# Kernel optimization log

Hardware: AMD Instinct MI355X
Metric: run time of the kernel (lower is better)

## Reference

```python
import jax, jax.numpy as jnp
import numpy as np

H = 12          # num_heads
E = 768         # key_dim
LORA_SCALE = 32.0 / 4.0  # scale / R
NEG = -1e9


def setup_inputs() -> dict:
    key = jax.random.key(0)
    ks = jax.random.split(key, 8)
    B, L = 2, 2048
    return {
        "x": jax.random.normal(ks[0], (B, L, E), jnp.float32),
        "w_in": jax.random.normal(ks[1], (E, 3 * E), jnp.float32) * 0.02,
        "b_in": jnp.zeros((3 * E,), jnp.float32),
        "A_in": jax.random.normal(ks[2], (4, 3 * E), jnp.float32) * 0.02,
        "B_in": jax.random.normal(ks[3], (E, 4), jnp.float32) * 0.02,
        "w_out": jax.random.normal(ks[4], (E, E), jnp.float32) * 0.02,
        "b_out": jnp.zeros((E,), jnp.float32),
        "A_out": jax.random.normal(ks[5], (4, E), jnp.float32) * 0.02,
        "B_out": jax.random.normal(ks[6], (E, 4), jnp.float32) * 0.02,
    }


def reference(x, w_in, b_in, A_in, B_in, w_out, b_out, A_out, B_out):
    Bb, L, _ = x.shape
    D = E // H
    # LoRA-adapted input projection: w + (scale/R) * B @ A
    w1 = w_in + LORA_SCALE * (B_in @ A_in)          # [E, 3E]
    c = jnp.einsum('ble,eo->blo', x, w1) + b_in      # [B, L, 3E]
    q, k, v = jnp.split(c, 3, axis=2)
    # split heads -> [B, H, L, D]
    def heads(t):
        return t.reshape(Bb, L, H, D).transpose(0, 2, 1, 3)
    q, k, v = heads(q), heads(k), heads(v)
    # attention scores (no 1/sqrt(d): scale=False in module defaults)
    w = jnp.einsum('bhqd,bhkd->bhqk', q, k)          # [B, H, L, L]
    band = jnp.tril(jnp.ones((L, L), jnp.float32))   # causal band
    w = w * band + NEG * (1.0 - band)
    w = jax.nn.softmax(w, axis=-1)
    a = jnp.einsum('bhqk,bhkd->bhqd', w, v)          # [B, H, L, D]
    a = a.transpose(0, 2, 1, 3).reshape(Bb, L, E)    # merge heads
    w2 = w_out + LORA_SCALE * (B_out @ A_out)        # [E, E]
    return jnp.einsum('ble,eo->blo', a, w2) + b_out
```

## Files before the change

kernel.cpp:

```cpp
#include <hip/hip_runtime.h>
#include <hip/hip_bf16.h>

#define BB 2
#define LL 2048
#define EE 768
#define HH 12
#define DD 64
#define N3 2304
#define TOK 4096
#define LOG2E 1.4426950408889634f

typedef __attribute__((ext_vector_type(8))) short short8;
typedef __attribute__((ext_vector_type(4))) float f32x4;
typedef __attribute__((ext_vector_type(4))) unsigned int uix4;
typedef unsigned int uint_t;
typedef unsigned short ushort_t;

__device__ __forceinline__ f32x4 mfma16(short8 a, short8 b, f32x4 c) {
  return __builtin_amdgcn_mfma_f32_16x16x32_bf16(a, b, c, 0, 0, 0);
}

__device__ __forceinline__ ushort_t bf16bits(float f) {
  __hip_bfloat16 h = __float2bfloat16(f);
  return *reinterpret_cast<ushort_t*>(&h);
}

__device__ __forceinline__ float bits2f(ushort_t u) {
  union { uint_t u; float f; } cv;
  cv.u = ((uint_t)u) << 16;
  return cv.f;
}

__device__ __forceinline__ void stage64(const __hip_bfloat16* gbase, int ldg,
                                        short* lds, int tid) {
  const int wave = tid >> 6, lane = tid & 63;
#pragma unroll
  for (int c = 0; c < 4; ++c) {
    int off = c * 4096 + wave * 1024 + lane * 16;
    int row = off >> 7;
    int cs  = (off & 127) >> 4;
    int cc  = cs ^ (row & 7);
    __builtin_amdgcn_global_load_lds(
        (const __attribute__((address_space(1))) void*)((const short*)gbase + (size_t)row * ldg + cc * 8),
        (__attribute__((address_space(3))) void*)(lds + c * 2048 + wave * 512),
        16, 0, 0);
  }
}

__device__ __forceinline__ void stage128(const __hip_bfloat16* gbase, int ldg,
                                         short* lds, int tid) {
  const int wave = tid >> 6, lane = tid & 63;
#pragma unroll
  for (int c = 0; c < 4; ++c) {
    int off = c * 4096 + wave * 1024 + lane * 16;
    int row = off >> 8;
    int cs  = (off & 255) >> 4;
    int cc  = cs ^ (row & 7);
    __builtin_amdgcn_global_load_lds(
        (const __attribute__((address_space(1))) void*)((const short*)gbase + (size_t)row * ldg + cc * 8),
        (__attribute__((address_space(3))) void*)(lds + c * 2048 + wave * 512),
        16, 0, 0);
  }
}

__device__ __forceinline__ short8 frag64(const short* lds, int row, int chunk) {
  return *(const short8*)(lds + row * 64 + (chunk ^ (row & 7)) * 8);
}
__device__ __forceinline__ short8 frag128(const short* lds, int row, int chunk) {
  return *(const short8*)(lds + row * 128 + (chunk ^ (row & 7)) * 8);
}

__global__ void prep_kernel(const float* __restrict__ x, const float* __restrict__ w_in,
                            const float* __restrict__ A_in, const float* __restrict__ B_in,
                            const float* __restrict__ w_out, const float* __restrict__ A_out,
                            const float* __restrict__ B_out,
                            __hip_bfloat16* __restrict__ xb, __hip_bfloat16* __restrict__ w1T,
                            __hip_bfloat16* __restrict__ w2T) {
  __shared__ float tile[32][33];
  const int bid = blockIdx.x, t = threadIdx.x;
  if (bid < 2304) {
    const float *W, *Am, *Bm;
    __hip_bfloat16* out;
    int N, tx, ty;
    if (bid < 1728) { W = w_in;  Am = A_in;  Bm = B_in;  out = w1T; N = N3; tx = bid % 72; ty = bid / 72; }
    else { int jj = bid - 1728; W = w_out; Am = A_out; Bm = B_out; out = w2T; N = EE; tx = jj % 24; ty = jj / 24; }
    const int e0 = ty * 32, o0 = tx * 32;
    const int r = t >> 5, col = t & 31;
#pragma unroll
    for (int i = 0; i < 4; ++i)
      tile[r + i * 8][col] = W[(size_t)(e0 + r + i * 8) * N + (o0 + col)];
    __syncthreads();
    const int e = e0 + col;
    const float b0 = Bm[e * 4 + 0], b1 = Bm[e * 4 + 1], b2 = Bm[e * 4 + 2], b3 = Bm[e * 4 + 3];
#pragma unroll
    for (int i = 0; i < 4; ++i) {
      const int o = o0 + r + i * 8;
      float acc = b0 * Am[o] + b1 * Am[N + o] + b2 * Am[2 * N + o] + b3 * Am[3 * N + o];
      out[(size_t)o * EE + e] = __float2bfloat16(tile[col][r + i * 8] + 8.0f * acc);
    }
  } else {
    const int j = bid - 2304;
    const float* src = x + (size_t)j * 4096 + t * 16;
    short* dst = (short*)xb + (size_t)j * 4096 + t * 16;
#pragma unroll
    for (int half = 0; half < 2; ++half) {
      float4 a = ((const float4*)src)[half * 2];
      float4 b = ((const float4*)src)[half * 2 + 1];
      short8 v;
      v[0] = (short)bf16bits(a.x); v[1] = (short)bf16bits(a.y);
      v[2] = (short)bf16bits(a.z); v[3] = (short)bf16bits(a.w);
      v[4] = (short)bf16bits(b.x); v[5] = (short)bf16bits(b.y);
      v[6] = (short)bf16bits(b.z); v[7] = (short)bf16bits(b.w);
      ((short8*)dst)[half] = v;
    }
  }
}

template<bool F32OUT, bool QSCALE>
__global__ __launch_bounds__(256, 2) void gemm_bt(const __hip_bfloat16* __restrict__ A,
                                                  const __hip_bfloat16* __restrict__ BT,
                                                  const float* __restrict__ bias,
                                                  void* __restrict__ outp,
                                                  int M, int N, int K) {
  __shared__ __align__(16) short Al[128 * 64];
  __shared__ __align__(16) short Bl[128 * 64];
  const int tid = threadIdx.x, lane = tid & 63, wave = tid >> 6;
  const int quad = lane >> 4, c16 = lane & 15;
  const int n0 = blockIdx.x * 128, m0 = blockIdx.y * 128;
  const int msub = (wave & 1) * 64, nsub = (wave >> 1) * 64;
  f32x4 acc[4][4] = {};
  for (int k0 = 0; k0 < K; k0 += 64) {
    __syncthreads();
    stage64(A + (size_t)m0 * K + k0, K, Al, tid);
    stage64(BT + (size_t)n0 * K + k0, K, Bl, tid);
    __syncthreads();
#pragma unroll
    for (int ks = 0; ks < 2; ++ks) {
      short8 af[4], bfr[4];
#pragma unroll
      for (int i = 0; i < 4; ++i) {
        af[i]  = frag64(Al, msub + i * 16 + c16, ks * 4 + quad);
        bfr[i] = frag64(Bl, nsub + i * 16 + c16, ks * 4 + quad);
      }
#pragma unroll
      for (int mi = 0; mi < 4; ++mi)
#pragma unroll
        for (int ni = 0; ni < 4; ++ni)
          acc[mi][ni] = mfma16(af[mi], bfr[ni], acc[mi][ni]);
    }
  }
#pragma unroll
  for (int ni = 0; ni < 4; ++ni) {
    int n = n0 + nsub + ni * 16 + c16;
    float bv = bias[n];
    float sc = (QSCALE && n < EE) ? LOG2E : 1.0f;
#pragma unroll
    for (int mi = 0; mi < 4; ++mi) {
      int row0 = m0 + msub + mi * 16 + quad * 4;
#pragma unroll
      for (int r = 0; r < 4; ++r) {
        float v = (acc[mi][ni][r] + bv) * sc;
        if (F32OUT) ((float*)outp)[(size_t)(row0 + r) * N + n] = v;
        else ((__hip_bfloat16*)outp)[(size_t)(row0 + r) * N + n] = __float2bfloat16(v);
      }
    }
  }
}

__global__ void vtrans_kernel(const __hip_bfloat16* __restrict__ qkv,
                              __hip_bfloat16* __restrict__ vT) {
  const int tid = threadIdx.x, lane = tid & 63, wave = tid >> 6;
  const int blk = blockIdx.x;
  const int bh = blk >> 6, lt = blk & 63;
  const int b = bh / HH, h = bh % HH;
  const int l0 = lt * 32 + wave * 8;
  const int i = lane >> 3, o = lane & 7;
  const short* src = (const short*)qkv + (size_t)(b * LL + l0 + i) * N3 + 2 * EE + h * DD + o * 8;
  uix4 u = *(const uix4*)src;
  {
    uix4 ov;
#pragma unroll
    for (int k = 0; k < 4; ++k) ov[k] = (uint_t)__shfl_xor((int)u[k], 8);
#pragma unroll
    for (int k = 0; k < 4; ++k)
      u[k] = ((i & 1) == 0) ? ((u[k] & 0xFFFFu) | (ov[k] << 16))
                            : ((ov[k] >> 16) | (u[k] & 0xFFFF0000u));
  }
  {
    uix4 ov;
#pragma unroll
    for (int k = 0; k < 4; ++k) ov[k] = (uint_t)__shfl_xor((int)u[k], 16);
    uint_t a0 = ((i & 2) == 0) ? u[0] : ov[1];
    uint_t a1 = ((i & 2) == 0) ? ov[0] : u[1];
    uint_t a2 = ((i & 2) == 0) ? u[2] : ov[3];
    uint_t a3 = ((i & 2) == 0) ? ov[2] : u[3];
    u[0] = a0; u[1] = a1; u[2] = a2; u[3] = a3;
  }
  {
    uix4 ov;
#pragma unroll
    for (int k = 0; k < 4; ++k) ov[k] = (uint_t)__shfl_xor((int)u[k], 32);
    uint_t a0 = ((i & 4) == 0) ? u[0] : ov[2];
    uint_t a1 = ((i & 4) == 0) ? u[1] : ov[3];
    uint_t a2 = ((i & 4) == 0) ? ov[0] : u[2];
    uint_t a3 = ((i & 4) == 0) ? ov[1] : u[3];
    u[0] = a0; u[1] = a1; u[2] = a2; u[3] = a3;
  }
  short* dst = (short*)vT + (size_t)((b * HH + h) * DD + o * 8 + i) * LL + l0;
  *(uix4*)dst = u;
}

#define SLOT_BYTES 8448
__global__ __launch_bounds__(256, 4) void attn_kernel(const __hip_bfloat16* __restrict__ qkv,
                                                      const __hip_bfloat16* __restrict__ vT,
                                                      char* __restrict__ Opart) {
  __shared__ __align__(16) short Kl[128 * 64];
  __shared__ __align__(16) short Vl[64 * 128];
  const int tid = threadIdx.x, lane = tid & 63, wave = tid >> 6;
  const int quad = lane >> 4, c16 = lane & 15;
  const int bid = blockIdx.x;
  const int bh = bid % 24;
  const int j = bid / 24;
  int qt, cch;
  if (j < 16)      { qt = 16 + j; cch = 0; }
  else if (j < 32) { qt = 47 - j; cch = 1; }
  else             { qt = 47 - j; cch = 0; }
  const int b = bh / HH, h = bh % HH;
  const int q0 = qt * 64;
  const int qw = q0 + wave * 16;
  const int ks = cch * 1024;
  const int ke = min((qt + 1) * 64, ks + 1024);
  short8 qf[2];
  {
    const short* qrow = (const short*)qkv + (size_t)(b * LL + qw + c16) * N3 + h * DD;
    qf[0] = *(const short8*)(qrow + quad * 8);
    qf[1] = *(const short8*)(qrow + 32 + quad * 8);
  }
  float l_i = 0.f;
  f32x4 oaccT[4] = {};
  const int srcA = ((lane >> 4) & 1) * 32 + c16;
  const int srcB = srcA + 16;
  const bool hi2 = (quad >> 1) != 0;
  for (int k0 = ks; k0 < ke; k0 += 128) {
    __syncthreads();
    stage64(qkv + (size_t)(b * LL + k0) * N3 + EE + h * DD, N3, Kl, tid);
    stage128(vT + (size_t)((b * HH + h) * DD) * LL + k0, LL, Vl, tid);
    __syncthreads();
    int nlim = (qw + 15 - k0) / 16 + 1;
    if (nlim > 8) nlim = 8;
    uint_t pkx[8], pky[8];
#pragma unroll
    for (int nt = 0; nt < 8; ++nt) {
      if (nt < nlim) {
        f32x4 a = {};
        a = mfma16(frag64(Kl, nt * 16 + c16, quad), qf[0], a);
        a = mfma16(frag64(Kl, nt * 16 + c16, 4 + quad), qf[1], a);
        if (k0 + nt * 16 + 15 > qw) {
          const int kb = k0 + nt * 16 + quad * 4;
          const int q = qw + c16;
#pragma unroll
          for (int r = 0; r < 4; ++r)
            if (kb + r > q) a[r] = -1e9f;
        }
        float p0 = exp2f(a[0]), p1 = exp2f(a[1]);
        float p2 = exp2f(a[2]), p3 = exp2f(a[3]);
        l_i += (p0 + p1) + (p2 + p3);
        pkx[nt] = (uint_t)bf16bits(p0) | ((uint_t)bf16bits(p1) << 16);
        pky[nt] = (uint_t)bf16bits(p2) | ((uint_t)bf16bits(p3) << 16);
      } else { pkx[nt] = 0; pky[nt] = 0; }
    }
    const int klim = (nlim + 1) >> 1;
#pragma unroll
    for (int kc = 0; kc < 4; ++kc) {
      if (kc < klim) {
        const int nt0 = 2 * kc, nt1 = 2 * kc + 1;
        uint_t a0 = (uint_t)__shfl((int)pkx[nt0], srcA);
        uint_t a1 = (uint_t)__shfl((int)pky[nt0], srcA);
        uint_t a2 = (uint_t)__shfl((int)pkx[nt0], srcB);
        uint_t a3 = (uint_t)__shfl((int)pky[nt0], srcB);
        uint_t b0 = (uint_t)__shfl((int)pkx[nt1], srcA);
        uint_t b1 = (uint_t)__shfl((int)pky[nt1], srcA);
        uint_t b2 = (uint_t)__shfl((int)pkx[nt1], srcB);
        uint_t b3 = (uint_t)__shfl((int)pky[nt1], srcB);
        union { uix4 u; short8 s8; } bf;
        bf.u[0] = hi2 ? b0 : a0;
        bf.u[1] = hi2 ? b1 : a1;
        bf.u[2] = hi2 ? b2 : a2;
        bf.u[3] = hi2 ? b3 : a3;
#pragma unroll
        for (int dt = 0; dt < 4; ++dt)
          oaccT[dt] = mfma16(frag128(Vl, dt * 16 + c16, kc * 4 + quad), bf.s8, oaccT[dt]);
      }
    }
  }
  float l_full = l_i;
  l_full += __shfl_xor(l_full, 16);
  l_full += __shfl_xor(l_full, 32);
  char* op = Opart + (size_t)((bh * 32 + qt) * 2 + cch) * SLOT_BYTES;
  __syncthreads();
  short* reg = Kl + wave * 1152;
#pragma unroll
  for (int dt = 0; dt < 4; ++dt) {
    uint_t w0 = (uint_t)bf16bits(oaccT[dt][0]) | ((uint_t)bf16bits(oaccT[dt][1]) << 16);
    uint_t w1 = (uint_t)bf16bits(oaccT[dt][2]) | ((uint_t)bf16bits(oaccT[dt][3]) << 16);
    uint_t* p = (uint_t*)(reg + c16 * 72 + dt * 16 + quad * 4);
    p[0] = w0; p[1] = w1;
  }
  if (quad == 0) ((float*)(op + 8192))[wave * 16 + c16] = l_full;
#pragma unroll
  for (int it = 0; it < 2; ++it) {
    int idx = it * 64 + lane;
    int tq = idx >> 3, c = idx & 7;
    short8 v = *(const short8*)(reg + tq * 72 + c * 8);
    *(short8*)((short*)op + (wave * 16 + tq) * 64 + c * 8) = v;
  }
}

__global__ void merge_kernel(const char* __restrict__ Opart,
                             __hip_bfloat16* __restrict__ abuf) {
  const int t = threadIdx.x;
  const int bh = blockIdx.x >> 5, qt = blockIdx.x & 31;
  const int b = bh / HH, h = bh % HH;
  const char* p0 = Opart + (size_t)((bh * 32 + qt) * 2) * SLOT_BYTES;
  const char* p1 = p0 + SLOT_BYTES;
  const bool two = (qt >= 16);
  const int q = t >> 2, dc = (t & 3) * 16;
  float l = ((const float*)(p0 + 8192))[q];
  if (two) l += ((const float*)(p1 + 8192))[q];
  const float inv = 1.0f / l;
  const short* o0 = (const short*)p0 + q * 64 + dc;
  const short* o1 = (const short*)p1 + q * 64 + dc;
  short8 r0[2], r1[2];
  r0[0] = *(const short8*)(o0);
  r0[1] = *(const short8*)(o0 + 8);
  if (two) { r1[0] = *(const short8*)(o1); r1[1] = *(const short8*)(o1 + 8); }
  __align__(16) short out[16];
#pragma unroll
  for (int i = 0; i < 16; ++i) {
    float v = bits2f((ushort_t)r0[i >> 3][i & 7]);
    if (two) v += bits2f((ushort_t)r1[i >> 3][i & 7]);
    out[i] = (short)bf16bits(v * inv);
  }
  short* dst = (short*)abuf + (size_t)(b * LL + qt * 64 + q) * EE + h * DD + dc;
  *(short8*)dst = *(short8*)(out);
  *(short8*)(dst + 8) = *(short8*)(out + 8);
}

extern "C" void kernel_launch(void* const* d_in, const int* in_sizes, int n_in,
                              void* d_out, int out_size, void* d_ws, size_t ws_size,
                              hipStream_t stream) {
  (void)in_sizes; (void)n_in; (void)out_size; (void)ws_size;
  const float* x     = (const float*)d_in[0];
  const float* w_in  = (const float*)d_in[1];
  const float* b_in  = (const float*)d_in[2];
  const float* A_in  = (const float*)d_in[3];
  const float* B_in  = (const float*)d_in[4];
  const float* w_out = (const float*)d_in[5];
  const float* b_out = (const float*)d_in[6];
  const float* A_out = (const float*)d_in[7];
  const float* B_out = (const float*)d_in[8];
  char* ws = (char*)d_ws;
  __hip_bfloat16* xb   = (__hip_bfloat16*)(ws);
  __hip_bfloat16* w1T  = (__hip_bfloat16*)(ws + 6291456);
  __hip_bfloat16* w2T  = (__hip_bfloat16*)(ws + 9830400);
  __hip_bfloat16* qkv  = (__hip_bfloat16*)(ws + 11010048);
  __hip_bfloat16* vT   = (__hip_bfloat16*)(ws + 29884416);
  __hip_bfloat16* abuf = (__hip_bfloat16*)(ws + 36175872);
  char* Opart          = ws + 42467328;

  prep_kernel<<<3072, 256, 0, stream>>>(x, w_in, A_in, B_in, w_out, A_out, B_out,
                                        xb, w1T, w2T);
  gemm_bt<false, true><<<dim3(N3 / 128, TOK / 128), 256, 0, stream>>>(xb, w1T, b_in, qkv, TOK, N3, EE);
  vtrans_kernel<<<BB * HH * 64, 256, 0, stream>>>(qkv, vT);
  attn_kernel<<<24 * 48, 256, 0, stream>>>(qkv, vT, Opart);
  merge_kernel<<<24 * 32, 256, 0, stream>>>(Opart, abuf);
  gemm_bt<true, false><<<dim3(EE / 128, TOK / 128), 256, 0, stream>>>(abuf, w2T, b_out, d_out, TOK, EE, EE);
}
```

Measured before the change: 171.8 us.

## Process 128-query tiles per block with two 16-row query groups per wave

The attention kernel now gives each wave 32 query rows as two 16-row sub-tiles, so each K and V fragment read from LDS is reused for both. Block count and merge grid are halved to match. The PV product now uses the 16x16x16 bf16 MFMA with P fed straight from registers, which removes the cross-lane shuffles that repacked P. In exchange there are fewer blocks to fill the GPU, more registers per wave, and causal imbalance inside each 128-row tile.

```diff
diff --git a/kernel.cpp b/kernel.cpp
--- a/kernel.cpp
+++ b/kernel.cpp
@@ -11,6 +11,7 @@
 #define LOG2E 1.4426950408889634f
 
 typedef __attribute__((ext_vector_type(8))) short short8;
+typedef __attribute__((ext_vector_type(4))) short s16x4;
 typedef __attribute__((ext_vector_type(4))) float f32x4;
 typedef __attribute__((ext_vector_type(4))) unsigned int uix4;
 typedef unsigned int uint_t;
@@ -18,6 +19,9 @@
 
 __device__ __forceinline__ f32x4 mfma16(short8 a, short8 b, f32x4 c) {
   return __builtin_amdgcn_mfma_f32_16x16x32_bf16(a, b, c, 0, 0, 0);
+}
+__device__ __forceinline__ f32x4 mfma16k16(s16x4 a, s16x4 b, f32x4 c) {
+  return __builtin_amdgcn_mfma_f32_16x16x16bf16_1k(a, b, c, 0, 0, 0);
 }
 
 __device__ __forceinline__ ushort_t bf16bits(float f) {
@@ -65,9 +69,6 @@
 
 __device__ __forceinline__ short8 frag64(const short* lds, int row, int chunk) {
   return *(const short8*)(lds + row * 64 + (chunk ^ (row & 7)) * 8);
-}
-__device__ __forceinline__ short8 frag128(const short* lds, int row, int chunk) {
-  return *(const short8*)(lds + row * 128 + (chunk ^ (row & 7)) * 8);
 }
 
 __global__ void prep_kernel(const float* __restrict__ x, const float* __restrict__ w_in,
@@ -210,7 +211,9 @@
   *(uix4*)dst = u;
 }
 
-#define SLOT_BYTES 8448
+#define SLOT_BYTES 16896
+union pk4 { uint_t u[2]; s16x4 s4; };
+
 __global__ __launch_bounds__(256, 4) void attn_kernel(const __hip_bfloat16* __restrict__ qkv,
                                                       const __hip_bfloat16* __restrict__ vT,
                                                       char* __restrict__ Opart) {
@@ -222,128 +225,150 @@
   const int bh = bid % 24;
   const int j = bid / 24;
   int qt, cch;
-  if (j < 16)      { qt = 16 + j; cch = 0; }
-  else if (j < 32) { qt = 47 - j; cch = 1; }
-  else             { qt = 47 - j; cch = 0; }
+  if (j < 8)       { qt = 8 + j;  cch = 0; }
+  else if (j < 16) { qt = 23 - j; cch = 1; }
+  else             { qt = 23 - j; cch = 0; }
   const int b = bh / HH, h = bh % HH;
-  const int q0 = qt * 64;
-  const int qw = q0 + wave * 16;
+  const int q0 = qt * 128;
+  const int qw = q0 + wave * 32;
   const int ks = cch * 1024;
-  const int ke = min((qt + 1) * 64, ks + 1024);
-  short8 qf[2];
+  const int ke = min(q0 + 128, ks + 1024);
+  short8 qfA[2], qfB[2];
   {
-    const short* qrow = (const short*)qkv + (size_t)(b * LL + qw + c16) * N3 + h * DD;
-    qf[0] = *(const short8*)(qrow + quad * 8);
-    qf[1] = *(const short8*)(qrow + 32 + quad * 8);
-  }
-  float l_i = 0.f;
-  f32x4 oaccT[4] = {};
-  const int srcA = ((lane >> 4) & 1) * 32 + c16;
-  const int srcB = srcA + 16;
-  const bool hi2 = (quad >> 1) != 0;
+    const short* qra = (const short*)qkv + (size_t)(b * LL + qw + c16) * N3 + h * DD;
+    qfA[0] = *(const short8*)(qra + quad * 8);
+    qfA[1] = *(const short8*)(qra + 32 + quad * 8);
+    const short* qrb = qra + 16 * N3;
+    qfB[0] = *(const short8*)(qrb + quad * 8);
+    qfB[1] = *(const short8*)(qrb + 32 + quad * 8);
+  }
+  float lA = 0.f, lB = 0.f;
+  f32x4 oA[4] = {}, oB[4] = {};
+  const int vsub = (quad & 1) * 4;
+  const int cxor = (c16 & 7);
   for (int k0 = ks; k0 < ke; k0 += 128) {
     __syncthreads();
     stage64(qkv + (size_t)(b * LL + k0) * N3 + EE + h * DD, N3, Kl, tid);
     stage128(vT + (size_t)((b * HH + h) * DD) * LL + k0, LL, Vl, tid);
     __syncthreads();
-    int nlim = (qw + 15 - k0) / 16 + 1;
-    if (nlim > 8) nlim = 8;
-    uint_t pkx[8], pky[8];
+    int nlimB = (qw + 31 - k0) / 16 + 1; if (nlimB > 8) nlimB = 8;
+    int nlimA = (qw + 15 - k0) / 16 + 1; if (nlimA > 8) nlimA = 8;
 #pragma unroll
     for (int nt = 0; nt < 8; ++nt) {
-      if (nt < nlim) {
-        f32x4 a = {};
-        a = mfma16(frag64(Kl, nt * 16 + c16, quad), qf[0], a);
-        a = mfma16(frag64(Kl, nt * 16 + c16, 4 + quad), qf[1], a);
-        if (k0 + nt * 16 + 15 > qw) {
-          const int kb = k0 + nt * 16 + quad * 4;
-          const int q = qw + c16;
+      if (nt < nlimB) {
+        const short* krow = Kl + (nt * 16 + c16) * 64;
+        const int kc0 = (quad ^ cxor) * 8;
+        short8 kf0 = *(const short8*)(krow + kc0);
+        short8 kf1 = *(const short8*)(krow + (kc0 ^ 32));
+        const int kb = k0 + nt * 16 + quad * 4;
+        const bool diag = (k0 + nt * 16 + 15 > qw + 16);
+        f32x4 sB = {};
+        sB = mfma16(kf0, qfB[0], sB);
+        sB = mfma16(kf1, qfB[1], sB);
+        if (diag) {
+          const int q = qw + 16 + c16;
 #pragma unroll
           for (int r = 0; r < 4; ++r)
-            if (kb + r > q) a[r] = -1e9f;
+            if (kb + r > q) sB[r] = -1e9f;
         }
-        float p0 = exp2f(a[0]), p1 = exp2f(a[1]);
-        float p2 = exp2f(a[2]), p3 = exp2f(a[3]);
-        l_i += (p0 + p1) + (p2 + p3);
-        pkx[nt] = (uint_t)bf16bits(p0) | ((uint_t)bf16bits(p1) << 16);
-        pky[nt] = (uint_t)bf16bits(p2) | ((uint_t)bf16bits(p3) << 16);
-      } else { pkx[nt] = 0; pky[nt] = 0; }
-    }
-    const int klim = (nlim + 1) >> 1;
-#pragma unroll
-    for (int kc = 0; kc < 4; ++kc) {
-      if (kc < klim) {
-        const int nt0 = 2 * kc, nt1 = 2 * kc + 1;
-        uint_t a0 = (uint_t)__shfl((int)pkx[nt0], srcA);
-        uint_t a1 = (uint_t)__shfl((int)pky[nt0], srcA);
-        uint_t a2 = (uint_t)__shfl((int)pkx[nt0], srcB);
-        uint_t a3 = (uint_t)__shfl((int)pky[nt0], srcB);
-        uint_t b0 = (uint_t)__shfl((int)pkx[nt1], srcA);
-        uint_t b1 = (uint_t)__shfl((int)pky[nt1], srcA);
-        uint_t b2 = (uint_t)__shfl((int)pkx[nt1], srcB);
-        uint_t b3 = (uint_t)__shfl((int)pky[nt1], srcB);
-        union { uix4 u; short8 s8; } bf;
-        bf.u[0] = hi2 ? b0 : a0;
-        bf.u[1] = hi2 ? b1 : a1;
-        bf.u[2] = hi2 ? b2 : a2;
-        bf.u[3] = hi2 ? b3 : a3;
-#pragma unroll
-        for (int dt = 0; dt < 4; ++dt)
-          oaccT[dt] = mfma16(frag128(Vl, dt * 16 + c16, kc * 4 + quad), bf.s8, oaccT[dt]);
+        pk4 pB;
+        {
+          float p0 = exp2f(sB[0]), p1 = exp2f(sB[1]);
+          float p2 = exp2f(sB[2]), p3 = exp2f(sB[3]);
+          lB += (p0 + p1) + (p2 + p3);
+          pB.u[0] = (uint_t)bf16bits(p0) | ((uint_t)bf16bits(p1) << 16);
+          pB.u[1] = (uint_t)bf16bits(p2) | ((uint_t)bf16bits(p3) << 16);
+        }
+        const bool doA = (nt < nlimA);
+        pk4 pA;
+        if (doA) {
+          f32x4 sA = {};
+          sA = mfma16(kf0, qfA[0], sA);
+          sA = mfma16(kf1, qfA[1], sA);
+          if (k0 + nt * 16 + 15 > qw) {
+            const int q = qw + c16;
+#pragma unroll
+            for (int r = 0; r < 4; ++r)
+              if (kb + r > q) sA[r] = -1e9f;
+          }
+          float p0 = exp2f(sA[0]), p1 = exp2f(sA[1]);
+          float p2 = exp2f(sA[2]), p3 = exp2f(sA[3]);
+          lA += (p0 + p1) + (p2 + p3);
+          pA.u[0] = (uint_t)bf16bits(p0) | ((uint_t)bf16bits(p1) << 16);
+          pA.u[1] = (uint_t)bf16bits(p2) | ((uint_t)bf16bits(p3) << 16);
+        }
+        const int cg = nt * 2 + (quad >> 1);
+        const short* vbase = Vl + c16 * 128 + ((cg ^ cxor) * 8 + vsub);
+#pragma unroll
+        for (int dt = 0; dt < 4; ++dt) {
+          s16x4 vf = *(const s16x4*)(vbase + dt * 2048);
+          oB[dt] = mfma16k16(vf, pB.s4, oB[dt]);
+          if (doA) oA[dt] = mfma16k16(vf, pA.s4, oA[dt]);
+        }
       }
     }
   }
-  float l_full = l_i;
-  l_full += __shfl_xor(l_full, 16);
-  l_full += __shfl_xor(l_full, 32);
-  char* op = Opart + (size_t)((bh * 32 + qt) * 2 + cch) * SLOT_BYTES;
+  lA += __shfl_xor(lA, 16); lA += __shfl_xor(lA, 32);
+  lB += __shfl_xor(lB, 16); lB += __shfl_xor(lB, 32);
+  char* op = Opart + (size_t)((bh * 16 + qt) * 2 + cch) * SLOT_BYTES;
+  float* lout = (float*)(op + 16384);
   __syncthreads();
+  if (quad == 0) {
+    lout[wave * 32 + c16] = lA;
+    lout[wave * 32 + 16 + c16] = lB;
+  }
   short* reg = Kl + wave * 1152;
 #pragma unroll
-  for (int dt = 0; dt < 4; ++dt) {
-    uint_t w0 = (uint_t)bf16bits(oaccT[dt][0]) | ((uint_t)bf16bits(oaccT[dt][1]) << 16);
-    uint_t w1 = (uint_t)bf16bits(oaccT[dt][2]) | ((uint_t)bf16bits(oaccT[dt][3]) << 16);
-    uint_t* p = (uint_t*)(reg + c16 * 72 + dt * 16 + quad * 4);
-    p[0] = w0; p[1] = w1;
-  }
-  if (quad == 0) ((float*)(op + 8192))[wave * 16 + c16] = l_full;
-#pragma unroll
-  for (int it = 0; it < 2; ++it) {
-    int idx = it * 64 + lane;
-    int tq = idx >> 3, c = idx & 7;
-    short8 v = *(const short8*)(reg + tq * 72 + c * 8);
-    *(short8*)((short*)op + (wave * 16 + tq) * 64 + c * 8) = v;
+  for (int hh = 0; hh < 2; ++hh) {
+#pragma unroll
+    for (int dt = 0; dt < 4; ++dt) {
+      f32x4 o = hh ? oB[dt] : oA[dt];
+      uint_t w0 = (uint_t)bf16bits(o[0]) | ((uint_t)bf16bits(o[1]) << 16);
+      uint_t w1 = (uint_t)bf16bits(o[2]) | ((uint_t)bf16bits(o[3]) << 16);
+      uint_t* p = (uint_t*)(reg + c16 * 72 + dt * 16 + quad * 4);
+      p[0] = w0; p[1] = w1;
+    }
+#pragma unroll
+    for (int it = 0; it < 2; ++it) {
+      int idx = it * 64 + lane;
+      int tq = idx >> 3, c = idx & 7;
+      short8 v = *(const short8*)(reg + tq * 72 + c * 8);
+      *(short8*)((short*)op + (wave * 32 + hh * 16 + tq) * 64 + c * 8) = v;
+    }
   }
 }
 
 __global__ void merge_kernel(const char* __restrict__ Opart,
                              __hip_bfloat16* __restrict__ abuf) {
   const int t = threadIdx.x;
-  const int bh = blockIdx.x >> 5, qt = blockIdx.x & 31;
+  const int bh = blockIdx.x >> 4, qt = blockIdx.x & 15;
   const int b = bh / HH, h = bh % HH;
-  const char* p0 = Opart + (size_t)((bh * 32 + qt) * 2) * SLOT_BYTES;
+  const char* p0 = Opart + (size_t)((bh * 16 + qt) * 2) * SLOT_BYTES;
   const char* p1 = p0 + SLOT_BYTES;
-  const bool two = (qt >= 16);
-  const int q = t >> 2, dc = (t & 3) * 16;
-  float l = ((const float*)(p0 + 8192))[q];
-  if (two) l += ((const float*)(p1 + 8192))[q];
+  const bool two = (qt >= 8);
+  const int q = t >> 1, dc = (t & 1) * 32;
+  float l = ((const float*)(p0 + 16384))[q];
+  if (two) l += ((const float*)(p1 + 16384))[q];
   const float inv = 1.0f / l;
   const short* o0 = (const short*)p0 + q * 64 + dc;
   const short* o1 = (const short*)p1 + q * 64 + dc;
-  short8 r0[2], r1[2];
-  r0[0] = *(const short8*)(o0);
-  r0[1] = *(const short8*)(o0 + 8);
-  if (two) { r1[0] = *(const short8*)(o1); r1[1] = *(const short8*)(o1 + 8); }
-  __align__(16) short out[16];
-#pragma unroll
-  for (int i = 0; i < 16; ++i) {
-    float v = bits2f((ushort_t)r0[i >> 3][i & 7]);
-    if (two) v += bits2f((ushort_t)r1[i >> 3][i & 7]);
-    out[i] = (short)bf16bits(v * inv);
-  }
-  short* dst = (short*)abuf + (size_t)(b * LL + qt * 64 + q) * EE + h * DD + dc;
-  *(short8*)dst = *(short8*)(out);
-  *(short8*)(dst + 8) = *(short8*)(out + 8);
+  __align__(16) short out[32];
+#pragma unroll
+  for (int blk = 0; blk < 4; ++blk) {
+    short8 r0 = *(const short8*)(o0 + blk * 8);
+    short8 r1;
+    if (two) r1 = *(const short8*)(o1 + blk * 8);
+#pragma unroll
+    for (int i = 0; i < 8; ++i) {
+      float v = bits2f((ushort_t)r0[i]);
+      if (two) v += bits2f((ushort_t)r1[i]);
+      out[blk * 8 + i] = (short)bf16bits(v * inv);
+    }
+  }
+  short* dst = (short*)abuf + (size_t)(b * LL + qt * 128 + q) * EE + h * DD + dc;
+#pragma unroll
+  for (int blk = 0; blk < 4; ++blk)
+    *(short8*)(dst + blk * 8) = *(short8*)(out + blk * 8);
 }
 
 extern "C" void kernel_launch(void* const* d_in, const int* in_sizes, int n_in,
@@ -372,7 +397,7 @@
                                         xb, w1T, w2T);
   gemm_bt<false, true><<<dim3(N3 / 128, TOK / 128), 256, 0, stream>>>(xb, w1T, b_in, qkv, TOK, N3, EE);
   vtrans_kernel<<<BB * HH * 64, 256, 0, stream>>>(qkv, vT);
-  attn_kernel<<<24 * 48, 256, 0, stream>>>(qkv, vT, Opart);
-  merge_kernel<<<24 * 32, 256, 0, stream>>>(Opart, abuf);
+  attn_kernel<<<24 * 24, 256, 0, stream>>>(qkv, vT, Opart);
+  merge_kernel<<<24 * 16, 256, 0, stream>>>(Opart, abuf);
   gemm_bt<true, false><<<dim3(EE / 128, TOK / 128), 256, 0, stream>>>(abuf, w2T, b_out, d_out, TOK, EE, EE);
 }
```

Result: no change. 172.7 us (+0.5%).
